# Optimization experiments

Hardware: AMD Instinct MI355X
Metric: run time of the kernel (lower is better)

## Reference

```python
import jax, jax.numpy as jnp
import numpy as np

N_NODES = 100000
N_EDGES = 1600000
D = 128  # 2 * config.out_channels with config.out_channels = 64


def setup_inputs() -> dict:
    key = jax.random.key(0)
    k1, k2, k3, k4 = jax.random.split(key, 4)
    x_in = jax.random.normal(k1, (N_NODES, D), dtype=jnp.float32)
    x_out = jax.random.normal(k2, (N_NODES, D), dtype=jnp.float32)
    edge_index = jax.random.randint(k3, (2, N_EDGES), 0, N_NODES, dtype=jnp.int64)
    # nn.Bilinear(D, D, 1, bias=False) weight: [out_features=1, D, D]
    W = jax.random.normal(k4, (1, D, D), dtype=jnp.float32) * (1.0 / np.sqrt(D))
    return {"x_in": x_in, "x_out": x_out, "edge_index": edge_index, "W": W}


def reference(x_in, x_out, edge_index, W):
    # Gather edge endpoint features (irregular access)
    a = x_out[edge_index[0]]          # [E, D]
    b = x_in[edge_index[1]]           # [E, D]
    # Bilinear form with single output: value_e = a_e^T W0 b_e
    W0 = W[0]                         # [D, D]
    aW = a @ W0                       # [E, D]
    value = jnp.sum(aW * b, axis=-1)  # [E]
    return jax.nn.sigmoid(value)
```

## Files before the change

kernel.cpp:

```cpp
#include <hip/hip_runtime.h>
#include <hip/hip_fp16.h>
#include <math.h>

#define D 128
#define TM 128
#define BKk 32
#define XPAD 4

typedef _Float16 h2_t __attribute__((ext_vector_type(2)));

__device__ __forceinline__ float dot2acc(unsigned ua, unsigned ub, float c) {
#if __has_builtin(__builtin_amdgcn_fdot2)
  return __builtin_amdgcn_fdot2(__builtin_bit_cast(h2_t, ua),
                                __builtin_bit_cast(h2_t, ub), c, false);
#else
  __half2 a = __builtin_bit_cast(__half2, ua);
  __half2 b = __builtin_bit_cast(__half2, ub);
  float2 fa = __half22float2(a), fb = __half22float2(b);
  return fmaf(fa.x, fb.x, fmaf(fa.y, fb.y, c));
#endif
}

__global__ __launch_bounds__(256) void convert_f16_kernel(
    const float* __restrict__ x, __half* __restrict__ xh, int n4)
{
  int i = blockIdx.x * 256 + threadIdx.x;
  if (i >= n4) return;
  float4 v = ((const float4*)x)[i];
  __half2 h0, h1;
  h0.x = __float2half_rn(v.x); h0.y = __float2half_rn(v.y);
  h1.x = __float2half_rn(v.z); h1.y = __float2half_rn(v.w);
  uint2 u;
  u.x = __builtin_bit_cast(unsigned, h0);
  u.y = __builtin_bit_cast(unsigned, h1);
  ((uint2*)xh)[i] = u;
}

__global__ __launch_bounds__(256) void gemm_xw_f16_kernel(
    const float* __restrict__ X, const float* __restrict__ W,
    __half* __restrict__ Y, int N)
{
  __shared__ __align__(16) float sX[BKk][TM + XPAD];
  __shared__ __align__(16) float sW[BKk][D];

  const int tid  = threadIdx.x;
  const int row0 = blockIdx.x * TM;
  const int tr   = tid >> 4;
  const int tc   = tid & 15;

  float acc[8][8];
  #pragma unroll
  for (int r = 0; r < 8; r++)
    #pragma unroll
    for (int c = 0; c < 8; c++) acc[r][c] = 0.0f;

  for (int k0 = 0; k0 < D; k0 += BKk) {
    {
      const float4* Wg  = (const float4*)(W + (size_t)k0 * D);
      float4*       sWv = (float4*)(&sW[0][0]);
      #pragma unroll
      for (int i = 0; i < 4; i++)
        sWv[tid + i * 256] = Wg[tid + i * 256];
    }
    {
      #pragma unroll
      for (int i = 0; i < 4; i++) {
        int idx = tid + i * 256;
        int kq  = idx & 7;
        int r   = idx >> 3;
        int grow = row0 + r;
        float4 v = make_float4(0.f, 0.f, 0.f, 0.f);
        if (grow < N)
          v = *(const float4*)(X + (size_t)grow * D + k0 + kq * 4);
        sX[kq * 4 + 0][r] = v.x;
        sX[kq * 4 + 1][r] = v.y;
        sX[kq * 4 + 2][r] = v.z;
        sX[kq * 4 + 3][r] = v.w;
      }
    }
    __syncthreads();

    #pragma unroll 8
    for (int k = 0; k < BKk; k++) {
      float a[8], w[8];
      *(float4*)&a[0] = *(const float4*)&sX[k][tr * 8];
      *(float4*)&a[4] = *(const float4*)&sX[k][tr * 8 + 4];
      *(float4*)&w[0] = *(const float4*)&sW[k][tc * 4];
      *(float4*)&w[4] = *(const float4*)&sW[k][64 + tc * 4];
      #pragma unroll
      for (int r = 0; r < 8; r++)
        #pragma unroll
        for (int c = 0; c < 8; c++)
          acc[r][c] = fmaf(a[r], w[c], acc[r][c]);
    }
    __syncthreads();
  }

  #pragma unroll
  for (int r = 0; r < 8; r++) {
    int grow = row0 + tr * 8 + r;
    if (grow < N) {
      __half* yrow = Y + (size_t)grow * D;
      __half2 h0, h1;
      h0.x = __float2half_rn(acc[r][0]); h0.y = __float2half_rn(acc[r][1]);
      h1.x = __float2half_rn(acc[r][2]); h1.y = __float2half_rn(acc[r][3]);
      uint2 u0;
      u0.x = __builtin_bit_cast(unsigned, h0);
      u0.y = __builtin_bit_cast(unsigned, h1);
      *(uint2*)(yrow + tc * 4) = u0;
      h0.x = __float2half_rn(acc[r][4]); h0.y = __float2half_rn(acc[r][5]);
      h1.x = __float2half_rn(acc[r][6]); h1.y = __float2half_rn(acc[r][7]);
      uint2 u1;
      u1.x = __builtin_bit_cast(unsigned, h0);
      u1.y = __builtin_bit_cast(unsigned, h1);
      *(uint2*)(yrow + 64 + tc * 4) = u1;
    }
  }
}

__global__ __launch_bounds__(256) void edge_dot_f16_kernel(
    const __half* __restrict__ Yh, const __half* __restrict__ Xh,
    const int* __restrict__ idx, float* __restrict__ out, int E)
{
  long long gid = (long long)blockIdx.x * 256 + threadIdx.x;
  int e = (int)(gid >> 4);
  if (e >= E) return;
  int l = (int)(gid & 15);

  int src = idx[e];
  int dst = idx[E + e];

  uint4 ya = ((const uint4*)(Yh + (size_t)src * D))[l];
  uint4 xb = ((const uint4*)(Xh + (size_t)dst * D))[l];

  float s = 0.0f;
  s = dot2acc(ya.x, xb.x, s);
  s = dot2acc(ya.y, xb.y, s);
  s = dot2acc(ya.z, xb.z, s);
  s = dot2acc(ya.w, xb.w, s);

  s += __shfl_xor(s, 8);
  s += __shfl_xor(s, 4);
  s += __shfl_xor(s, 2);
  s += __shfl_xor(s, 1);

  if (l == 0)
    out[e] = 1.0f / (1.0f + __expf(-s));
}

__global__ __launch_bounds__(256) void edge_bilinear_direct_kernel(
    const float* __restrict__ Xout, const float* __restrict__ Xin,
    const float* __restrict__ W, const int* __restrict__ idx,
    float* __restrict__ out, int E)
{
  long long gid = (long long)blockIdx.x * 256 + threadIdx.x;
  int e = (int)(gid >> 6);
  if (e >= E) return;
  int l = (int)(gid & 63);

  int src = idx[e];
  int dst = idx[E + e];
  const float* a = Xout + (size_t)src * D;
  const float* b = Xin  + (size_t)dst * D;

  float s = 0.f;
  #pragma unroll
  for (int kk = 0; kk < 2; kk++) {
    int k = l + kk * 64;
    float ak = a[k];
    float t = 0.f;
    const float* wr = W + (size_t)k * D;
    #pragma unroll 8
    for (int j = 0; j < D; j++) t = fmaf(wr[j], b[j], t);
    s = fmaf(ak, t, s);
  }
  #pragma unroll
  for (int off = 32; off >= 1; off >>= 1) s += __shfl_xor(s, off);
  if (l == 0) out[e] = 1.0f / (1.0f + __expf(-s));
}

extern "C" void kernel_launch(void* const* d_in, const int* in_sizes, int n_in,
                              void* d_out, int out_size, void* d_ws, size_t ws_size,
                              hipStream_t stream) {
  const float* x_in  = (const float*)d_in[0];
  const float* x_out = (const float*)d_in[1];
  const int*   eidx  = (const int*)d_in[2];
  const float* W     = (const float*)d_in[3];
  float* out = (float*)d_out;

  const int N = in_sizes[0] / D;
  const int E = in_sizes[2] / 2;

  size_t half_rows = (size_t)N * D * sizeof(__half);

  if (ws_size >= 2 * half_rows) {
    __half* Yh = (__half*)d_ws;
    __half* Xh = (__half*)((char*)d_ws + half_rows);

    int n4 = N * D / 4;
    convert_f16_kernel<<<(n4 + 255) / 256, 256, 0, stream>>>(x_in, Xh, n4);

    dim3 g1((N + TM - 1) / TM);
    gemm_xw_f16_kernel<<<g1, 256, 0, stream>>>(x_out, W, Yh, N);

    long long total = (long long)E * 16;
    dim3 g2((unsigned)((total + 255) / 256));
    edge_dot_f16_kernel<<<g2, 256, 0, stream>>>(Yh, Xh, eidx, out, E);
  } else {
    long long total = (long long)E * 64;
    dim3 g((unsigned)((total + 255) / 256));
    edge_bilinear_direct_kernel<<<g, 256, 0, stream>>>(x_out, x_in, W, eidx, out, E);
  }
}
```

Baseline: 284.5 us.

## Use MFMA f16 GEMM for x_out@W and process two edges per lane group

Replaces the scalar fp32 FMA GEMM with an MFMA 16x16x32 f16 kernel. It pre-transposes W to fp16, stages X and Wt in swizzled LDS, and writes Y with per-element half stores. The edge kernel now handles two edges per 16-lane group, which doubles loads in flight per thread and vectorizes the output store. It adds a small transpose kernel and may use d_out as scratch for Wt when the workspace is too small. It also rounds W to fp16, which changes numerics slightly.

```diff
diff --git a/kernel.cpp b/kernel.cpp
--- a/kernel.cpp
+++ b/kernel.cpp
@@ -3,11 +3,10 @@
 #include <math.h>
 
 #define D 128
-#define TM 128
-#define BKk 32
-#define XPAD 4
-
-typedef _Float16 h2_t __attribute__((ext_vector_type(2)));
+
+typedef _Float16 f16x8 __attribute__((ext_vector_type(8)));
+typedef float    f32x4 __attribute__((ext_vector_type(4)));
+typedef _Float16 h2_t  __attribute__((ext_vector_type(2)));
 
 __device__ __forceinline__ float dot2acc(unsigned ua, unsigned ub, float c) {
 #if __has_builtin(__builtin_amdgcn_fdot2)
@@ -21,131 +20,159 @@
 #endif
 }
 
+__device__ __forceinline__ unsigned pack2(float x, float y) {
+  __half2 h;
+  h.x = __float2half_rn(x);
+  h.y = __float2half_rn(y);
+  return __builtin_bit_cast(unsigned, h);
+}
+
 __global__ __launch_bounds__(256) void convert_f16_kernel(
     const float* __restrict__ x, __half* __restrict__ xh, int n4)
 {
   int i = blockIdx.x * 256 + threadIdx.x;
   if (i >= n4) return;
   float4 v = ((const float4*)x)[i];
-  __half2 h0, h1;
-  h0.x = __float2half_rn(v.x); h0.y = __float2half_rn(v.y);
-  h1.x = __float2half_rn(v.z); h1.y = __float2half_rn(v.w);
   uint2 u;
-  u.x = __builtin_bit_cast(unsigned, h0);
-  u.y = __builtin_bit_cast(unsigned, h1);
+  u.x = pack2(v.x, v.y);
+  u.y = pack2(v.z, v.w);
   ((uint2*)xh)[i] = u;
 }
 
-__global__ __launch_bounds__(256) void gemm_xw_f16_kernel(
-    const float* __restrict__ X, const float* __restrict__ W,
+__global__ __launch_bounds__(256) void transpose_w_kernel(
+    const float* __restrict__ W, __half* __restrict__ Wt)
+{
+  int o = blockIdx.x * 256 + threadIdx.x;
+  if (o >= D * D) return;
+  int k = o >> 7;
+  int n = o & 127;
+  Wt[n * D + k] = __float2half_rn(W[o]);
+}
+
+__global__ __launch_bounds__(256) void gemm_mfma_kernel(
+    const float* __restrict__ X, const __half* __restrict__ Wt,
     __half* __restrict__ Y, int N)
 {
-  __shared__ __align__(16) float sX[BKk][TM + XPAD];
-  __shared__ __align__(16) float sW[BKk][D];
+  __shared__ __align__(16) __half sA[128 * 128];
+  __shared__ __align__(16) __half sB[128 * 128];
 
   const int tid  = threadIdx.x;
-  const int row0 = blockIdx.x * TM;
-  const int tr   = tid >> 4;
-  const int tc   = tid & 15;
-
-  float acc[8][8];
-  #pragma unroll
-  for (int r = 0; r < 8; r++)
-    #pragma unroll
-    for (int c = 0; c < 8; c++) acc[r][c] = 0.0f;
-
-  for (int k0 = 0; k0 < D; k0 += BKk) {
-    {
-      const float4* Wg  = (const float4*)(W + (size_t)k0 * D);
-      float4*       sWv = (float4*)(&sW[0][0]);
+  const int row0 = blockIdx.x * 128;
+
+  #pragma unroll
+  for (int i = 0; i < 16; i++) {
+    int idx = tid + i * 256;
+    int q   = idx & 31;
+    int r   = idx >> 5;
+    int gr  = row0 + r;
+    float4 v = make_float4(0.f, 0.f, 0.f, 0.f);
+    if (gr < N) v = *(const float4*)(X + (size_t)gr * D + q * 4);
+    uint2 u;
+    u.x = pack2(v.x, v.y);
+    u.y = pack2(v.z, v.w);
+    int g   = q >> 1;
+    int sub = q & 1;
+    int off = r * 128 + (((g + r) & 15) << 3) + (sub << 2);
+    *(uint2*)(sA + off) = u;
+  }
+  #pragma unroll
+  for (int i = 0; i < 8; i++) {
+    int idx = tid + i * 256;
+    int g   = idx & 15;
+    int n   = idx >> 4;
+    uint4 v = *(const uint4*)(Wt + n * 128 + g * 8);
+    int off = n * 128 + (((g + n) & 15) << 3);
+    *(uint4*)(sB + off) = v;
+  }
+  __syncthreads();
+
+  const int wave = tid >> 6;
+  const int lane = tid & 63;
+  const int m    = lane & 15;
+  const int quad = lane >> 4;
+
+  f32x4 acc[2][8];
+  #pragma unroll
+  for (int rt = 0; rt < 2; rt++)
+    #pragma unroll
+    for (int ct = 0; ct < 8; ct++)
+      acc[rt][ct] = (f32x4){0.f, 0.f, 0.f, 0.f};
+
+  #pragma unroll
+  for (int ks = 0; ks < 4; ks++) {
+    const int g = ks * 4 + quad;
+    f16x8 bfrag[8];
+    #pragma unroll
+    for (int ct = 0; ct < 8; ct++) {
+      int n = ct * 16 + m;
+      bfrag[ct] = *(const f16x8*)(sB + n * 128 + (((g + n) & 15) << 3));
+    }
+    #pragma unroll
+    for (int rt = 0; rt < 2; rt++) {
+      int r = wave * 32 + rt * 16 + m;
+      f16x8 afrag = *(const f16x8*)(sA + r * 128 + (((g + r) & 15) << 3));
       #pragma unroll
-      for (int i = 0; i < 4; i++)
-        sWv[tid + i * 256] = Wg[tid + i * 256];
+      for (int ct = 0; ct < 8; ct++)
+        acc[rt][ct] = __builtin_amdgcn_mfma_f32_16x16x32_f16(
+            afrag, bfrag[ct], acc[rt][ct], 0, 0, 0);
     }
-    {
-      #pragma unroll
-      for (int i = 0; i < 4; i++) {
-        int idx = tid + i * 256;
-        int kq  = idx & 7;
-        int r   = idx >> 3;
-        int grow = row0 + r;
-        float4 v = make_float4(0.f, 0.f, 0.f, 0.f);
-        if (grow < N)
-          v = *(const float4*)(X + (size_t)grow * D + k0 + kq * 4);
-        sX[kq * 4 + 0][r] = v.x;
-        sX[kq * 4 + 1][r] = v.y;
-        sX[kq * 4 + 2][r] = v.z;
-        sX[kq * 4 + 3][r] = v.w;
+  }
+
+  #pragma unroll
+  for (int rt = 0; rt < 2; rt++) {
+    #pragma unroll
+    for (int reg = 0; reg < 4; reg++) {
+      int gr = row0 + wave * 32 + rt * 16 + quad * 4 + reg;
+      if (gr < N) {
+        __half* yrow = Y + (size_t)gr * D;
+        #pragma unroll
+        for (int ct = 0; ct < 8; ct++)
+          yrow[ct * 16 + m] = __float2half_rn(acc[rt][ct][reg]);
       }
     }
-    __syncthreads();
-
-    #pragma unroll 8
-    for (int k = 0; k < BKk; k++) {
-      float a[8], w[8];
-      *(float4*)&a[0] = *(const float4*)&sX[k][tr * 8];
-      *(float4*)&a[4] = *(const float4*)&sX[k][tr * 8 + 4];
-      *(float4*)&w[0] = *(const float4*)&sW[k][tc * 4];
-      *(float4*)&w[4] = *(const float4*)&sW[k][64 + tc * 4];
-      #pragma unroll
-      for (int r = 0; r < 8; r++)
-        #pragma unroll
-        for (int c = 0; c < 8; c++)
-          acc[r][c] = fmaf(a[r], w[c], acc[r][c]);
-    }
-    __syncthreads();
-  }
-
-  #pragma unroll
-  for (int r = 0; r < 8; r++) {
-    int grow = row0 + tr * 8 + r;
-    if (grow < N) {
-      __half* yrow = Y + (size_t)grow * D;
-      __half2 h0, h1;
-      h0.x = __float2half_rn(acc[r][0]); h0.y = __float2half_rn(acc[r][1]);
-      h1.x = __float2half_rn(acc[r][2]); h1.y = __float2half_rn(acc[r][3]);
-      uint2 u0;
-      u0.x = __builtin_bit_cast(unsigned, h0);
-      u0.y = __builtin_bit_cast(unsigned, h1);
-      *(uint2*)(yrow + tc * 4) = u0;
-      h0.x = __float2half_rn(acc[r][4]); h0.y = __float2half_rn(acc[r][5]);
-      h1.x = __float2half_rn(acc[r][6]); h1.y = __float2half_rn(acc[r][7]);
-      uint2 u1;
-      u1.x = __builtin_bit_cast(unsigned, h0);
-      u1.y = __builtin_bit_cast(unsigned, h1);
-      *(uint2*)(yrow + 64 + tc * 4) = u1;
-    }
-  }
-}
-
-__global__ __launch_bounds__(256) void edge_dot_f16_kernel(
+  }
+}
+
+__global__ __launch_bounds__(256) void edge_dot2_kernel(
     const __half* __restrict__ Yh, const __half* __restrict__ Xh,
     const int* __restrict__ idx, float* __restrict__ out, int E)
 {
   long long gid = (long long)blockIdx.x * 256 + threadIdx.x;
-  int e = (int)(gid >> 4);
-  if (e >= E) return;
-  int l = (int)(gid & 15);
-
-  int src = idx[e];
-  int dst = idx[E + e];
-
-  uint4 ya = ((const uint4*)(Yh + (size_t)src * D))[l];
-  uint4 xb = ((const uint4*)(Xh + (size_t)dst * D))[l];
-
-  float s = 0.0f;
-  s = dot2acc(ya.x, xb.x, s);
-  s = dot2acc(ya.y, xb.y, s);
-  s = dot2acc(ya.z, xb.z, s);
-  s = dot2acc(ya.w, xb.w, s);
-
-  s += __shfl_xor(s, 8);
-  s += __shfl_xor(s, 4);
-  s += __shfl_xor(s, 2);
-  s += __shfl_xor(s, 1);
-
-  if (l == 0)
-    out[e] = 1.0f / (1.0f + __expf(-s));
+  int slot = (int)(gid >> 4);
+  int l    = (int)(gid & 15);
+  int e0 = slot * 2;
+  if (e0 >= E) return;
+  int e1 = e0 + 1;
+  bool has1 = (e1 < E);
+
+  int s0 = idx[e0];
+  int d0 = idx[E + e0];
+  int s1 = has1 ? idx[e1] : s0;
+  int d1 = has1 ? idx[E + e1] : d0;
+
+  uint4 a0 = ((const uint4*)(Yh + (size_t)s0 * D))[l];
+  uint4 b0 = ((const uint4*)(Xh + (size_t)d0 * D))[l];
+  uint4 a1 = ((const uint4*)(Yh + (size_t)s1 * D))[l];
+  uint4 b1 = ((const uint4*)(Xh + (size_t)d1 * D))[l];
+
+  float p = 0.f, q = 0.f;
+  p = dot2acc(a0.x, b0.x, p);  q = dot2acc(a1.x, b1.x, q);
+  p = dot2acc(a0.y, b0.y, p);  q = dot2acc(a1.y, b1.y, q);
+  p = dot2acc(a0.z, b0.z, p);  q = dot2acc(a1.z, b1.z, q);
+  p = dot2acc(a0.w, b0.w, p);  q = dot2acc(a1.w, b1.w, q);
+
+  p += __shfl_xor(p, 8);  q += __shfl_xor(q, 8);
+  p += __shfl_xor(p, 4);  q += __shfl_xor(q, 4);
+  p += __shfl_xor(p, 2);  q += __shfl_xor(q, 2);
+  p += __shfl_xor(p, 1);  q += __shfl_xor(q, 1);
+
+  if (l == 0) {
+    float2 o;
+    o.x = 1.0f / (1.0f + __expf(-p));
+    o.y = 1.0f / (1.0f + __expf(-q));
+    if (has1) *(float2*)(out + e0) = o;
+    else      out[e0] = o.x;
+  }
 }
 
 __global__ __launch_bounds__(256) void edge_bilinear_direct_kernel(
@@ -169,9 +196,8 @@
     int k = l + kk * 64;
     float ak = a[k];
     float t = 0.f;
-    const float* wr = W + (size_t)k * D;
     #pragma unroll 8
-    for (int j = 0; j < D; j++) t = fmaf(wr[j], b[j], t);
+    for (int j = 0; j < D; j++) t = fmaf(W[(size_t)k * D + j], b[j], t);
     s = fmaf(ak, t, s);
   }
   #pragma unroll
@@ -191,21 +217,29 @@
   const int N = in_sizes[0] / D;
   const int E = in_sizes[2] / 2;
 
-  size_t half_rows = (size_t)N * D * sizeof(__half);
+  const size_t half_rows = (size_t)N * D * sizeof(__half);
 
   if (ws_size >= 2 * half_rows) {
     __half* Yh = (__half*)d_ws;
     __half* Xh = (__half*)((char*)d_ws + half_rows);
+    __half* Wt;
+    if (ws_size >= 2 * half_rows + (size_t)D * D * sizeof(__half))
+      Wt = (__half*)((char*)d_ws + 2 * half_rows);
+    else
+      Wt = (__half*)d_out;
 
     int n4 = N * D / 4;
     convert_f16_kernel<<<(n4 + 255) / 256, 256, 0, stream>>>(x_in, Xh, n4);
 
-    dim3 g1((N + TM - 1) / TM);
-    gemm_xw_f16_kernel<<<g1, 256, 0, stream>>>(x_out, W, Yh, N);
-
-    long long total = (long long)E * 16;
+    transpose_w_kernel<<<(D * D + 255) / 256, 256, 0, stream>>>(W, Wt);
+
+    dim3 g1((N + 127) / 128);
+    gemm_mfma_kernel<<<g1, 256, 0, stream>>>(x_out, Wt, Yh, N);
+
+    long long slots = (E + 1) / 2;
+    long long total = slots * 16;
     dim3 g2((unsigned)((total + 255) / 256));
-    edge_dot_f16_kernel<<<g2, 256, 0, stream>>>(Yh, Xh, eidx, out, E);
+    edge_dot2_kernel<<<g2, 256, 0, stream>>>(Yh, Xh, eidx, out, E);
   } else {
     long long total = (long long)E * 64;
     dim3 g((unsigned)((total + 255) / 256));
```

New measurement: 259.3 us. -8.9%, faster.
